# Optimization experiments

Hardware: AMD Instinct MI355X
Metric: run time of the kernel (lower is better)

## Reference

```python
import jax, jax.numpy as jnp
import numpy as np

B, L, H, HEADS = 2, 2048, 1024, 16
D = H // HEADS  # head_dim = 64


def _rel_pos_bias(q, pos_emb):
    """Skewing trick: q is (b,h,L,d) (already scaled), pos_emb is (2L-1,d).
    Returns relative positional bias of shape (b,h,L,L)."""
    b, h, l, _ = q.shape
    p = jnp.einsum('bhid,jd->bhij', q, pos_emb)          # (b,h,L,2L-1)
    p = jnp.pad(p, ((0, 0), (0, 0), (0, 0), (0, 1)))     # (b,h,L,2L)
    p = p.reshape(b, h, l * 2 * l)                        # flatten last two dims
    p = jnp.pad(p, ((0, 0), (0, 0), (0, l - 1)))          # append L-1 zeros
    p = p.reshape(b, h, l + 1, 2 * l - 1)
    return p[:, :, :-1, -l:]                              # (b,h,L,L)


def setup_inputs() -> dict:
    key = jax.random.key(0)
    ks = jax.random.split(key, 12)
    s = 1.0 / np.sqrt(H)
    inp = {
        'query': jax.random.normal(ks[0], (B, L, H), jnp.float32),
        'key':   jax.random.normal(ks[1], (B, L, H), jnp.float32),
        'value': jax.random.normal(ks[2], (B, L, H), jnp.float32),
        'Wq_w': jax.random.normal(ks[3], (H, H), jnp.float32) * s,
        'Wq_b': jnp.zeros((H,), jnp.float32),
        'Wk_w': jax.random.normal(ks[4], (H, H), jnp.float32) * s,
        'Wk_b': jnp.zeros((H,), jnp.float32),
        'Wv_w': jax.random.normal(ks[5], (H, H), jnp.float32) * s,
        'Wv_b': jnp.zeros((H,), jnp.float32),
        'Wo_w': jax.random.normal(ks[6], (H, H), jnp.float32) * s,
        'Wo_b': jnp.zeros((H,), jnp.float32),
        'pos_emb': jax.random.normal(ks[7], (2 * L - 1, D), jnp.float32),
    }
    return inp


def reference(query, key, value, Wq_w, Wq_b, Wk_w, Wk_b, Wv_w, Wv_b, Wo_w, Wo_b, pos_emb):
    b = query.shape[0]
    q = query @ Wq_w.T + Wq_b
    k = key @ Wk_w.T + Wk_b
    v = value @ Wv_w.T + Wv_b
    # (b,L,h*d) -> (b,h,L,d)
    split = lambda x: x.reshape(b, L, HEADS, D).transpose(0, 2, 1, 3)
    q, k, v = split(q), split(k), split(v)
    q = q / np.sqrt(D)  # note: scaled q is also used for positional bias (faithful)
    attn = jnp.einsum('bhid,bhjd->bhij', q, k)
    attn = attn + _rel_pos_bias(q, pos_emb)
    causal = jnp.triu(jnp.full((L, L), -jnp.inf, jnp.float32), k=1)
    attn = attn + causal  # broadcasts over (b,h)
    score = jax.nn.softmax(attn, axis=-1)
    out = jnp.einsum('bhqk,bhkd->bhqd', score, v)
    out = out.transpose(0, 2, 1, 3).reshape(b, L, H)
    return out @ Wo_w.T + Wo_b
```

## Files before the change

### kernel.cpp

```cpp
#include <hip/hip_runtime.h>

#define L_SEQ 2048
#define NH    16
#define HD    64
#define HDIM  1024

typedef __attribute__((ext_vector_type(8))) short  short8;
typedef __attribute__((ext_vector_type(4))) float  f32x4;

__device__ __forceinline__ unsigned short f2bf(float f) {
    unsigned int u = __float_as_uint(f);
    u += 0x7fffu + ((u >> 16) & 1u);
    return (unsigned short)(u >> 16);
}

__device__ __forceinline__ short8 ld8(const unsigned short* p) {
    return *(const short8*)p;
}

__device__ __forceinline__ unsigned int cvtpk(float a, float b) {
    unsigned int r;
    asm("v_cvt_pk_bf16_f32 %0, %1, %2" : "=v"(r) : "v"(a), "v"(b));
    return r;
}

__device__ __forceinline__ void gl16(const unsigned short* g, unsigned short* l) {
    __builtin_amdgcn_global_load_lds(
        (const __attribute__((address_space(1))) void*)g,
        (__attribute__((address_space(3))) void*)l, 16, 0, 0);
}

__global__ __launch_bounds__(256) void cvt_a_kernel(
    const float* __restrict__ q, const float* __restrict__ k,
    const float* __restrict__ Wq, const float* __restrict__ Wk,
    const float* __restrict__ Wv, const float* __restrict__ Wo,
    const float* __restrict__ pe,
    unsigned short* __restrict__ S1, unsigned short* __restrict__ Vb,
    unsigned short* __restrict__ D, unsigned short* __restrict__ E)
{
    const int y = blockIdx.y;
    const float* src; unsigned short* dst; int n8;
    switch (y) {
        case 0:  src = q;  dst = S1;            n8 = 524288; break;
        case 1:  src = k;  dst = Vb;            n8 = 524288; break;
        case 2:  src = Wq; dst = D;             n8 = 131072; break;
        case 3:  src = Wk; dst = D + 1048576;   n8 = 131072; break;
        case 4:  src = Wv; dst = D + 2097152;   n8 = 131072; break;
        case 5:  src = Wo; dst = D + 3145728;   n8 = 131072; break;
        default: src = pe; dst = E;             n8 = 32760;  break;
    }
    const int i = blockIdx.x * 256 + threadIdx.x;
    if (i >= n8) return;
    const float4 a = ((const float4*)src)[2 * i];
    const float4 b = ((const float4*)src)[2 * i + 1];
    union { short8 v; unsigned int u[4]; } o;
    o.u[0] = cvtpk(a.x, a.y); o.u[1] = cvtpk(a.z, a.w);
    o.u[2] = cvtpk(b.x, b.y); o.u[3] = cvtpk(b.z, b.w);
    ((short8*)dst)[i] = o.v;
}

__global__ __launch_bounds__(256) void cvt_x_kernel(const float* __restrict__ src,
                                                    unsigned short* __restrict__ dst) {
    const int i = blockIdx.x * 256 + threadIdx.x;
    const float4 a = ((const float4*)src)[2 * i];
    const float4 b = ((const float4*)src)[2 * i + 1];
    union { short8 v; unsigned int u[4]; } o;
    o.u[0] = cvtpk(a.x, a.y); o.u[1] = cvtpk(a.z, a.w);
    o.u[2] = cvtpk(b.x, b.y); o.u[3] = cvtpk(b.z, b.w);
    ((short8*)dst)[i] = o.v;
}

__device__ __forceinline__ void gemm_bf16_core(
    const unsigned short* __restrict__ Xb,
    const unsigned short* __restrict__ Wb,
    int row0, int col0,
    unsigned short* As, unsigned short* Bs,
    f32x4 (&acc)[4][4])
{
    const int t    = threadIdx.x;
    const int lane = t & 63;
    const int wid  = t >> 6;
    const int lr   = lane & 15;
    const int lg   = lane >> 4;
    const int wr   = (wid >> 1) << 6;
    const int wc   = (wid & 1) << 6;

    const int grow = lane >> 3;
    const int gcol = ((lane & 7) ^ grow) << 3;

#pragma unroll
    for (int m = 0; m < 4; ++m)
#pragma unroll
        for (int n = 0; n < 4; ++n)
            acc[m][n] = (f32x4)0.0f;

    const unsigned short* xs = Xb + (size_t)(row0 + grow) * 1024 + gcol;
    const unsigned short* ws = Wb + (size_t)(col0 + grow) * 1024 + gcol;

    for (int k0 = 0; k0 < 1024; k0 += 64) {
        __syncthreads();
#pragma unroll
        for (int i = 0; i < 4; ++i) {
            const int seg = (i << 2) + wid;
            gl16(xs + (size_t)(seg << 3) * 1024 + k0, As + seg * 512);
            gl16(ws + (size_t)(seg << 3) * 1024 + k0, Bs + seg * 512);
        }
        __syncthreads();

        short8 af[4][2], bf[4][2];
#pragma unroll
        for (int m = 0; m < 4; ++m) {
            const int row = wr + (m << 4) + lr;
#pragma unroll
            for (int h = 0; h < 2; ++h)
                af[m][h] = ld8(&As[row * 64 + ((((h << 2) + lg) ^ (lr & 7)) << 3)]);
        }
#pragma unroll
        for (int n = 0; n < 4; ++n) {
            const int row = wc + (n << 4) + lr;
#pragma unroll
            for (int h = 0; h < 2; ++h)
                bf[n][h] = ld8(&Bs[row * 64 + ((((h << 2) + lg) ^ (lr & 7)) << 3)]);
        }
#pragma unroll
        for (int m = 0; m < 4; ++m)
#pragma unroll
            for (int n = 0; n < 4; ++n) {
                acc[m][n] = __builtin_amdgcn_mfma_f32_16x16x32_bf16(af[m][0], bf[n][0], acc[m][n], 0, 0, 0);
                acc[m][n] = __builtin_amdgcn_mfma_f32_16x16x32_bf16(af[m][1], bf[n][1], acc[m][n], 0, 0, 0);
            }
    }
}

__global__ __launch_bounds__(256) void proj_qk_kernel(
    const unsigned short* __restrict__ Xq, const unsigned short* __restrict__ Xk,
    const unsigned short* __restrict__ D,
    const float* __restrict__ bq, const float* __restrict__ bk,
    unsigned short* __restrict__ Qb, unsigned short* __restrict__ Kb)
{
    __shared__ __align__(16) unsigned short As[128 * 64];
    __shared__ __align__(16) unsigned short Bs[128 * 64];

    const int z = blockIdx.x >> 8;
    const int d = blockIdx.x & 255;
    const int y = ((d >> 6) << 3) | (d & 7);
    const int x = (d >> 3) & 7;
    const int row0 = y << 7, col0 = x << 7;

    const unsigned short* Xb = z ? Xk : Xq;
    const unsigned short* Wb = D + (z ? 1048576 : 0);
    const float* bias = z ? bk : bq;
    unsigned short* out = z ? Kb : Qb;
    const float scale = z ? 1.0f : 0.125f;

    f32x4 acc[4][4];
    gemm_bf16_core(Xb, Wb, row0, col0, As, Bs, acc);

    const int t = threadIdx.x;
    const int lane = t & 63;
    const int wid  = t >> 6;
    const int lr = lane & 15, lg = lane >> 4;
    const int wr = (wid >> 1) << 6, wc = (wid & 1) << 6;

#pragma unroll
    for (int n = 0; n < 4; ++n) {
        const int o = col0 + wc + (n << 4) + lr;
        const float bo = bias[o];
        const int h = o >> 6, dd = o & 63;
#pragma unroll
        for (int m = 0; m < 4; ++m) {
            const int ib = row0 + wr + (m << 4) + (lg << 2);
#pragma unroll
            for (int r = 0; r < 4; ++r) {
                const int i = ib + r;
                out[(((size_t)((i >> 11) * NH + h)) * L_SEQ + (i & (L_SEQ - 1))) * HD + dd] =
                    f2bf((acc[m][n][r] + bo) * scale);
            }
        }
    }
}

__global__ __launch_bounds__(256) void proj_v_kernel(
    const unsigned short* __restrict__ Xb, const unsigned short* __restrict__ Wb,
    const float* __restrict__ bias, unsigned short* __restrict__ out)
{
    __shared__ __align__(16) unsigned short As[128 * 64];
    __shared__ __align__(16) unsigned short Bs[128 * 64];

    const int d = blockIdx.x;
    const int y = ((d >> 6) << 3) | (d & 7);
    const int x = (d >> 3) & 7;
    const int row0 = y << 7, col0 = x << 7;

    f32x4 acc[4][4];
    gemm_bf16_core(Xb, Wb, row0, col0, As, Bs, acc);

    const int t = threadIdx.x;
    const int lane = t & 63;
    const int wid  = t >> 6;
    const int lr = lane & 15, lg = lane >> 4;
    const int wr = (wid >> 1) << 6, wc = (wid & 1) << 6;

#pragma unroll
    for (int n = 0; n < 4; ++n) {
        const int o = col0 + wc + (n << 4) + lr;
        const float bo = bias[o];
        const int h = o >> 6, dd = o & 63;
#pragma unroll
        for (int m = 0; m < 4; ++m) {
            const int ib = row0 + wr + (m << 4) + (lg << 2);
            const int b = ib >> 11, il = ib & (L_SEQ - 1);
            ushort4 pk;
            pk.x = f2bf(acc[m][n][0] + bo);
            pk.y = f2bf(acc[m][n][1] + bo);
            pk.z = f2bf(acc[m][n][2] + bo);
            pk.w = f2bf(acc[m][n][3] + bo);
            *(ushort4*)&out[(((size_t)(b * NH + h)) * HD + dd) * L_SEQ + il] = pk;
        }
    }
}

__global__ __launch_bounds__(256) void outproj_kernel(
    const unsigned short* __restrict__ Ob, const unsigned short* __restrict__ Wb,
    const float* __restrict__ bias, float* __restrict__ Yout)
{
    __shared__ __align__(16) unsigned short As[128 * 64];
    __shared__ __align__(16) unsigned short Bs[128 * 64];

    const int d = blockIdx.x;
    const int y = ((d >> 6) << 3) | (d & 7);
    const int x = (d >> 3) & 7;
    const int row0 = y << 7, col0 = x << 7;

    f32x4 acc[4][4];
    gemm_bf16_core(Ob, Wb, row0, col0, As, Bs, acc);

    const int t = threadIdx.x;
    const int lane = t & 63;
    const int wid  = t >> 6;
    const int lr = lane & 15, lg = lane >> 4;
    const int wr = (wid >> 1) << 6, wc = (wid & 1) << 6;

#pragma unroll
    for (int n = 0; n < 4; ++n) {
        const int o = col0 + wc + (n << 4) + lr;
        const float bo = bias[o];
#pragma unroll
        for (int m = 0; m < 4; ++m) {
            const int ib = row0 + wr + (m << 4) + (lg << 2);
#pragma unroll
            for (int r = 0; r < 4; ++r)
                Yout[(size_t)(ib + r) * HDIM + o] = acc[m][n][r] + bo;
        }
    }
}

__device__ __forceinline__ void stage_kv(
    const unsigned short* __restrict__ kbase, const unsigned short* __restrict__ vbase,
    int j0, unsigned short (*Ksb)[64], unsigned short (*Vsb)[64], int wid, int lane)
{
    const int r8 = lane >> 3;
    const int gc = ((lane & 7) ^ r8) << 3;
#pragma unroll
    for (int s = 0; s < 2; ++s) {
        const int rw = (wid << 4) + (s << 3);
        gl16(kbase + (size_t)(j0 + rw + r8) * HD + gc, &Ksb[rw][0]);
        gl16(vbase + (size_t)(rw + r8) * L_SEQ + j0 + gc, &Vsb[rw][0]);
    }
}

__global__ __launch_bounds__(256, 3) void attn_kernel(
    const unsigned short* __restrict__ Q,
    const unsigned short* __restrict__ Kt,
    const unsigned short* __restrict__ VT,
    const unsigned short* __restrict__ PE,
    unsigned short* __restrict__ O)
{
    __shared__ __align__(16) unsigned short Ks[2][64][64];
    __shared__ __align__(16) unsigned short Vs[2][64][64];
    __shared__ __align__(16) float blds_all[4][64][20];

    const int t    = threadIdx.x;
    const int wid  = t >> 6;
    const int lane = t & 63;
    const int lr   = lane & 15;
    const int lg   = lane >> 4;
    const int lk   = lg << 3;

    const int p   = blockIdx.x;
    const int bh  = p & 31;
    const int rb  = 31 - (p >> 5);
    const int i0  = rb << 6;
    const int i0w = i0 + (wid << 4);
    const int nt  = rb + 1;

    const unsigned short* kbase = Kt + (size_t)bh * L_SEQ * HD;
    const unsigned short* vbase = VT + (size_t)bh * HD * L_SEQ;

    float (*blds)[20] = blds_all[wid];

    const unsigned short* qb = Q + ((size_t)bh * L_SEQ + i0w + lr) * HD + lk;
    const short8 aq0 = ld8(qb);
    const short8 aq1 = ld8(qb + 32);

    const int gi    = i0w + lr;
    const int idx0  = ((lg & 1) << 7) + (lr << 2);
    const int idx1  = idx0 + 64;
    const int selhi = lg >> 1;

    f32x4 oacc[4];
#pragma unroll
    for (int dt = 0; dt < 4; ++dt) oacc[dt] = (f32x4)0.0f;
    float mrun = -__builtin_inff();
    float lrun = 0.0f;

    const int jend = i0w + 15;

    f32x4 pqc = (f32x4)0.0f;
    {
        const unsigned short* pp = PE + (size_t)(2032 - i0w + lr) * HD + lk;
        pqc = __builtin_amdgcn_mfma_f32_16x16x32_bf16(aq0, ld8(pp), pqc, 0, 0, 0);
        pqc = __builtin_amdgcn_mfma_f32_16x16x32_bf16(aq1, ld8(pp + 32), pqc, 0, 0, 0);
    }

    stage_kv(kbase, vbase, 0, Ks[0], Vs[0], wid, lane);
    __syncthreads();

    int cur = 0;
    for (int tt = 0; tt < nt; ++tt) {
        const int j0   = tt << 6;
        const bool more = (tt + 1 < nt);

        if (more)
            stage_kv(kbase, vbase, j0 + 64, Ks[cur ^ 1], Vs[cur ^ 1], wid, lane);

        if (j0 <= jend) {
            f32x4 s2[4];
#pragma unroll
            for (int ct = 0; ct < 4; ++ct) {
                const int row = (ct << 4) + lr;
                const short8 k0 = *(const short8*)&Ks[cur][row][(lg ^ (lr & 7)) << 3];
                const short8 k1 = *(const short8*)&Ks[cur][row][((4 + lg) ^ (lr & 7)) << 3];
                f32x4 a = (f32x4)0.0f;
                a = __builtin_amdgcn_mfma_f32_16x16x32_bf16(k0, aq0, a, 0, 0, 0);
                a = __builtin_amdgcn_mfma_f32_16x16x32_bf16(k1, aq1, a, 0, 0, 0);
                s2[ct] = a;
            }

            const int mlo = 2032 + j0 - i0w;
            f32x4 pq[5];
            pq[0] = pqc;
#pragma unroll
            for (int pt = 1; pt < 5; ++pt) {
                f32x4 a = (f32x4)0.0f;
                const unsigned short* pp = PE + (size_t)(mlo + (pt << 4) + lr) * HD + lk;
                a = __builtin_amdgcn_mfma_f32_16x16x32_bf16(aq0, ld8(pp), a, 0, 0, 0);
                a = __builtin_amdgcn_mfma_f32_16x16x32_bf16(aq1, ld8(pp + 32), a, 0, 0, 0);
                pq[pt] = a;
            }
            pqc = pq[4];

#pragma unroll
            for (int r = 0; r < 4; ++r) {
                const int qw = (lg << 2) + r;
                {
                    const int kr = lr + qw - 15;
                    if (kr >= 0) blds[kr][qw] = pq[0][r];
                }
#pragma unroll
                for (int pt = 1; pt < 4; ++pt)
                    blds[(pt << 4) + lr + qw - 15][qw] = pq[pt][r];
                {
                    const int kr = 49 + lr + qw;
                    if (kr < 64) blds[kr][qw] = pq[4][r];
                }
            }

#pragma unroll
            for (int ct = 0; ct < 4; ++ct)
#pragma unroll
                for (int r = 0; r < 4; ++r) {
                    const int krl = (ct << 4) + (lg << 2) + r;
                    const float v = s2[ct][r] + blds[krl][lr];
                    s2[ct][r] = (j0 + krl > gi) ? -__builtin_inff() : v;
                }

            float c0 = fmaxf(fmaxf(s2[0][0], s2[0][1]), fmaxf(s2[0][2], s2[0][3]));
            float c1 = fmaxf(fmaxf(s2[1][0], s2[1][1]), fmaxf(s2[1][2], s2[1][3]));
            float c2 = fmaxf(fmaxf(s2[2][0], s2[2][1]), fmaxf(s2[2][2], s2[2][3]));
            float c3 = fmaxf(fmaxf(s2[3][0], s2[3][1]), fmaxf(s2[3][2], s2[3][3]));
            float vmax = fmaxf(fmaxf(c0, c1), fmaxf(c2, c3));
            vmax = fmaxf(vmax, __shfl_xor(vmax, 16));
            vmax = fmaxf(vmax, __shfl_xor(vmax, 32));
            const float mnew = fmaxf(mrun, vmax);
            const float sc = __expf(mrun - mnew);
            mrun = mnew;
#pragma unroll
            for (int ct = 0; ct < 4; ++ct)
#pragma unroll
                for (int r = 0; r < 4; ++r)
                    s2[ct][r] = __expf(s2[ct][r] - mnew);
            float t0 = (s2[0][0] + s2[0][1]) + (s2[0][2] + s2[0][3]);
            float t1 = (s2[1][0] + s2[1][1]) + (s2[1][2] + s2[1][3]);
            float t2 = (s2[2][0] + s2[2][1]) + (s2[2][2] + s2[2][3]);
            float t3 = (s2[3][0] + s2[3][1]) + (s2[3][2] + s2[3][3]);
            float sum = (t0 + t1) + (t2 + t3);
            sum += __shfl_xor(sum, 16);
            sum += __shfl_xor(sum, 32);
            lrun = lrun * sc + sum;
#pragma unroll
            for (int dt = 0; dt < 4; ++dt)
#pragma unroll
                for (int r = 0; r < 4; ++r)
                    oacc[dt][r] *= sc;

            unsigned int pkl[4], pkh[4];
#pragma unroll
            for (int ct = 0; ct < 4; ++ct) {
                pkl[ct] = cvtpk(s2[ct][0], s2[ct][1]);
                pkh[ct] = cvtpk(s2[ct][2], s2[ct][3]);
            }
            union { short8 v; int u[4]; } pf0, pf1;
#pragma unroll
            for (int m = 0; m < 4; ++m) {
                const int bidx = (m & 2) ? idx1 : idx0;
                const int a0 = __builtin_amdgcn_ds_bpermute(bidx, (int)((m & 1) ? pkh[0] : pkl[0]));
                const int a1 = __builtin_amdgcn_ds_bpermute(bidx, (int)((m & 1) ? pkh[1] : pkl[1]));
                pf0.u[m] = selhi ? a1 : a0;
                const int b0 = __builtin_amdgcn_ds_bpermute(bidx, (int)((m & 1) ? pkh[2] : pkl[2]));
                const int b1 = __builtin_amdgcn_ds_bpermute(bidx, (int)((m & 1) ? pkh[3] : pkl[3]));
                pf1.u[m] = selhi ? b1 : b0;
            }

#pragma unroll
            for (int dt = 0; dt < 4; ++dt) {
                const int row = (dt << 4) + lr;
                const short8 v0 = *(const short8*)&Vs[cur][row][(lg ^ (lr & 7)) << 3];
                const short8 v1 = *(const short8*)&Vs[cur][row][((4 + lg) ^ (lr & 7)) << 3];
                oacc[dt] = __builtin_amdgcn_mfma_f32_16x16x32_bf16(v0, pf0.v, oacc[dt], 0, 0, 0);
                oacc[dt] = __builtin_amdgcn_mfma_f32_16x16x32_bf16(v1, pf1.v, oacc[dt], 0, 0, 0);
            }
        }

        __syncthreads();
        cur ^= 1;
    }

    const float inv = 1.0f / lrun;
    const int b = bh >> 4, h = bh & 15;
#pragma unroll
    for (int dt = 0; dt < 4; ++dt) {
        uint2 u;
        u.x = cvtpk(oacc[dt][0] * inv, oacc[dt][1] * inv);
        u.y = cvtpk(oacc[dt][2] * inv, oacc[dt][3] * inv);
        *(uint2*)&O[((size_t)b * L_SEQ + i0w + lr) * HDIM + (h << 6) + (dt << 4) + (lg << 2)] = u;
    }
}

extern "C" void kernel_launch(void* const* d_in, const int* in_sizes, int n_in,
                              void* d_out, int out_size, void* d_ws, size_t ws_size,
                              hipStream_t stream) {
    (void)in_sizes; (void)n_in; (void)out_size;

    const float* query   = (const float*)d_in[0];
    const float* key_    = (const float*)d_in[1];
    const float* value   = (const float*)d_in[2];
    const float* Wq_w    = (const float*)d_in[3];
    const float* Wq_b    = (const float*)d_in[4];
    const float* Wk_w    = (const float*)d_in[5];
    const float* Wk_b    = (const float*)d_in[6];
    const float* Wv_w    = (const float*)d_in[7];
    const float* Wv_b    = (const float*)d_in[8];
    const float* Wo_w    = (const float*)d_in[9];
    const float* Wo_b    = (const float*)d_in[10];
    const float* pos_emb = (const float*)d_in[11];

    char* ws = (char*)d_ws;
    const size_t MB = 1024 * 1024;
    unsigned short* S1 = (unsigned short*)(ws);
    unsigned short* Qb = (unsigned short*)(ws + 8  * MB);
    unsigned short* Kb = (unsigned short*)(ws + 16 * MB);
    unsigned short* Vb = (unsigned short*)(ws + 24 * MB);
    unsigned short* D  = (unsigned short*)(ws + 32 * MB);
    unsigned short* E  = (unsigned short*)(ws + 40 * MB);

    const int npe = (2 * L_SEQ - 1) * HD;
    if (ws_size < (size_t)40 * MB + (size_t)npe * 2) return;

    cvt_a_kernel<<<dim3(2048, 7), 256, 0, stream>>>(query, key_, Wq_w, Wk_w, Wv_w, Wo_w,
                                                    pos_emb, S1, Vb, D, E);
    proj_qk_kernel<<<512, 256, 0, stream>>>(S1, Vb, D, Wq_b, Wk_b, Qb, Kb);
    cvt_x_kernel<<<2048, 256, 0, stream>>>(value, S1);
    proj_v_kernel<<<256, 256, 0, stream>>>(S1, D + 2097152, Wv_b, Vb);
    attn_kernel<<<1024, 256, 0, stream>>>(Qb, Kb, Vb, E, S1);
    outproj_kernel<<<256, 256, 0, stream>>>(S1, D + 3145728, Wo_b, (float*)d_out);
}
```

Measured before the change: 179.5 us.

## Fuse V projection into QK launch, add lazy softmax rescale and exp2

The value-input conversion is folded into the main conversion launch and the V projection into the Q/K projection launch. This removes two kernel launches and lets the three GEMMs fill the device together, using the output buffer as scratch for bf16 V and transposed V. In attention, Q is prescaled by log2(e) so the softmax uses exp2. The running-max rescale is skipped unless the max grows by more than a threshold, and the causal mask is applied only on diagonal tiles. The lazy rescale relies on fp32 headroom and adds a wave-wide vote.

```diff
diff --git a/kernel.cpp b/kernel.cpp
--- a/kernel.cpp
+++ b/kernel.cpp
@@ -31,11 +31,12 @@
 }
 
 __global__ __launch_bounds__(256) void cvt_a_kernel(
-    const float* __restrict__ q, const float* __restrict__ k,
+    const float* __restrict__ q, const float* __restrict__ k, const float* __restrict__ v,
     const float* __restrict__ Wq, const float* __restrict__ Wk,
     const float* __restrict__ Wv, const float* __restrict__ Wo,
     const float* __restrict__ pe,
     unsigned short* __restrict__ S1, unsigned short* __restrict__ Vb,
+    unsigned short* __restrict__ VSCR,
     unsigned short* __restrict__ D, unsigned short* __restrict__ E)
 {
     const int y = blockIdx.y;
@@ -47,7 +48,8 @@
         case 3:  src = Wk; dst = D + 1048576;   n8 = 131072; break;
         case 4:  src = Wv; dst = D + 2097152;   n8 = 131072; break;
         case 5:  src = Wo; dst = D + 3145728;   n8 = 131072; break;
-        default: src = pe; dst = E;             n8 = 32760;  break;
+        case 6:  src = pe; dst = E;             n8 = 32760;  break;
+        default: src = v;  dst = VSCR;          n8 = 524288; break;
     }
     const int i = blockIdx.x * 256 + threadIdx.x;
     if (i >= n8) return;
@@ -59,17 +61,6 @@
     ((short8*)dst)[i] = o.v;
 }
 
-__global__ __launch_bounds__(256) void cvt_x_kernel(const float* __restrict__ src,
-                                                    unsigned short* __restrict__ dst) {
-    const int i = blockIdx.x * 256 + threadIdx.x;
-    const float4 a = ((const float4*)src)[2 * i];
-    const float4 b = ((const float4*)src)[2 * i + 1];
-    union { short8 v; unsigned int u[4]; } o;
-    o.u[0] = cvtpk(a.x, a.y); o.u[1] = cvtpk(a.z, a.w);
-    o.u[2] = cvtpk(b.x, b.y); o.u[3] = cvtpk(b.z, b.w);
-    ((short8*)dst)[i] = o.v;
-}
-
 __device__ __forceinline__ void gemm_bf16_core(
     const unsigned short* __restrict__ Xb,
     const unsigned short* __restrict__ Wb,
@@ -132,11 +123,12 @@
     }
 }
 
-__global__ __launch_bounds__(256) void proj_qk_kernel(
+__global__ __launch_bounds__(256) void proj_qkv_kernel(
     const unsigned short* __restrict__ Xq, const unsigned short* __restrict__ Xk,
-    const unsigned short* __restrict__ D,
-    const float* __restrict__ bq, const float* __restrict__ bk,
-    unsigned short* __restrict__ Qb, unsigned short* __restrict__ Kb)
+    const unsigned short* __restrict__ Xv, const unsigned short* __restrict__ D,
+    const float* __restrict__ bq, const float* __restrict__ bk, const float* __restrict__ bv,
+    unsigned short* __restrict__ Qb, unsigned short* __restrict__ Kb,
+    unsigned short* __restrict__ VT)
 {
     __shared__ __align__(16) unsigned short As[128 * 64];
     __shared__ __align__(16) unsigned short Bs[128 * 64];
@@ -147,11 +139,9 @@
     const int x = (d >> 3) & 7;
     const int row0 = y << 7, col0 = x << 7;
 
-    const unsigned short* Xb = z ? Xk : Xq;
-    const unsigned short* Wb = D + (z ? 1048576 : 0);
-    const float* bias = z ? bk : bq;
-    unsigned short* out = z ? Kb : Qb;
-    const float scale = z ? 1.0f : 0.125f;
+    const unsigned short* Xb = (z == 0) ? Xq : (z == 1) ? Xk : Xv;
+    const unsigned short* Wb = D + (size_t)z * 1048576;
+    const float* bias = (z == 0) ? bq : (z == 1) ? bk : bv;
 
     f32x4 acc[4][4];
     gemm_bf16_core(Xb, Wb, row0, col0, As, Bs, acc);
@@ -162,60 +152,42 @@
     const int lr = lane & 15, lg = lane >> 4;
     const int wr = (wid >> 1) << 6, wc = (wid & 1) << 6;
 
-#pragma unroll
-    for (int n = 0; n < 4; ++n) {
-        const int o = col0 + wc + (n << 4) + lr;
-        const float bo = bias[o];
-        const int h = o >> 6, dd = o & 63;
-#pragma unroll
-        for (int m = 0; m < 4; ++m) {
-            const int ib = row0 + wr + (m << 4) + (lg << 2);
-#pragma unroll
-            for (int r = 0; r < 4; ++r) {
-                const int i = ib + r;
-                out[(((size_t)((i >> 11) * NH + h)) * L_SEQ + (i & (L_SEQ - 1))) * HD + dd] =
-                    f2bf((acc[m][n][r] + bo) * scale);
-            }
-        }
-    }
-}
-
-__global__ __launch_bounds__(256) void proj_v_kernel(
-    const unsigned short* __restrict__ Xb, const unsigned short* __restrict__ Wb,
-    const float* __restrict__ bias, unsigned short* __restrict__ out)
-{
-    __shared__ __align__(16) unsigned short As[128 * 64];
-    __shared__ __align__(16) unsigned short Bs[128 * 64];
-
-    const int d = blockIdx.x;
-    const int y = ((d >> 6) << 3) | (d & 7);
-    const int x = (d >> 3) & 7;
-    const int row0 = y << 7, col0 = x << 7;
-
-    f32x4 acc[4][4];
-    gemm_bf16_core(Xb, Wb, row0, col0, As, Bs, acc);
-
-    const int t = threadIdx.x;
-    const int lane = t & 63;
-    const int wid  = t >> 6;
-    const int lr = lane & 15, lg = lane >> 4;
-    const int wr = (wid >> 1) << 6, wc = (wid & 1) << 6;
-
-#pragma unroll
-    for (int n = 0; n < 4; ++n) {
-        const int o = col0 + wc + (n << 4) + lr;
-        const float bo = bias[o];
-        const int h = o >> 6, dd = o & 63;
-#pragma unroll
-        for (int m = 0; m < 4; ++m) {
-            const int ib = row0 + wr + (m << 4) + (lg << 2);
-            const int b = ib >> 11, il = ib & (L_SEQ - 1);
-            ushort4 pk;
-            pk.x = f2bf(acc[m][n][0] + bo);
-            pk.y = f2bf(acc[m][n][1] + bo);
-            pk.z = f2bf(acc[m][n][2] + bo);
-            pk.w = f2bf(acc[m][n][3] + bo);
-            *(ushort4*)&out[(((size_t)(b * NH + h)) * HD + dd) * L_SEQ + il] = pk;
+    if (z <= 1) {
+        const float scale = (z == 0) ? 0.125f * 1.44269504088896340736f : 1.0f;
+        unsigned short* out = (z == 0) ? Qb : Kb;
+#pragma unroll
+        for (int n = 0; n < 4; ++n) {
+            const int o = col0 + wc + (n << 4) + lr;
+            const float bo = bias[o];
+            const int h = o >> 6, dd = o & 63;
+#pragma unroll
+            for (int m = 0; m < 4; ++m) {
+                const int ib = row0 + wr + (m << 4) + (lg << 2);
+#pragma unroll
+                for (int r = 0; r < 4; ++r) {
+                    const int i = ib + r;
+                    out[(((size_t)((i >> 11) * NH + h)) * L_SEQ + (i & (L_SEQ - 1))) * HD + dd] =
+                        f2bf((acc[m][n][r] + bo) * scale);
+                }
+            }
+        }
+    } else {
+#pragma unroll
+        for (int n = 0; n < 4; ++n) {
+            const int o = col0 + wc + (n << 4) + lr;
+            const float bo = bias[o];
+            const int h = o >> 6, dd = o & 63;
+#pragma unroll
+            for (int m = 0; m < 4; ++m) {
+                const int ib = row0 + wr + (m << 4) + (lg << 2);
+                const int b = ib >> 11, il = ib & (L_SEQ - 1);
+                ushort4 pk;
+                pk.x = f2bf(acc[m][n][0] + bo);
+                pk.y = f2bf(acc[m][n][1] + bo);
+                pk.z = f2bf(acc[m][n][2] + bo);
+                pk.w = f2bf(acc[m][n][3] + bo);
+                *(ushort4*)&VT[(((size_t)(b * NH + h)) * HD + dd) * L_SEQ + il] = pk;
+            }
         }
     }
 }
@@ -376,14 +348,24 @@
                 }
             }
 
-#pragma unroll
-            for (int ct = 0; ct < 4; ++ct)
-#pragma unroll
-                for (int r = 0; r < 4; ++r) {
-                    const int krl = (ct << 4) + (lg << 2) + r;
-                    const float v = s2[ct][r] + blds[krl][lr];
-                    s2[ct][r] = (j0 + krl > gi) ? -__builtin_inff() : v;
-                }
+            if (j0 + 63 > i0w) {
+#pragma unroll
+                for (int ct = 0; ct < 4; ++ct)
+#pragma unroll
+                    for (int r = 0; r < 4; ++r) {
+                        const int krl = (ct << 4) + (lg << 2) + r;
+                        const float v = s2[ct][r] + blds[krl][lr];
+                        s2[ct][r] = (j0 + krl > gi) ? -__builtin_inff() : v;
+                    }
+            } else {
+#pragma unroll
+                for (int ct = 0; ct < 4; ++ct)
+#pragma unroll
+                    for (int r = 0; r < 4; ++r) {
+                        const int krl = (ct << 4) + (lg << 2) + r;
+                        s2[ct][r] += blds[krl][lr];
+                    }
+            }
 
             float c0 = fmaxf(fmaxf(s2[0][0], s2[0][1]), fmaxf(s2[0][2], s2[0][3]));
             float c1 = fmaxf(fmaxf(s2[1][0], s2[1][1]), fmaxf(s2[1][2], s2[1][3]));
@@ -392,14 +374,22 @@
             float vmax = fmaxf(fmaxf(c0, c1), fmaxf(c2, c3));
             vmax = fmaxf(vmax, __shfl_xor(vmax, 16));
             vmax = fmaxf(vmax, __shfl_xor(vmax, 32));
-            const float mnew = fmaxf(mrun, vmax);
-            const float sc = __expf(mrun - mnew);
-            mrun = mnew;
+            if (!__all(vmax <= mrun + 8.0f)) {
+                const float mnew = fmaxf(mrun, vmax);
+                const float sc = __builtin_amdgcn_exp2f(mrun - mnew);
+                mrun = mnew;
+                lrun *= sc;
+#pragma unroll
+                for (int dt = 0; dt < 4; ++dt)
+#pragma unroll
+                    for (int r = 0; r < 4; ++r)
+                        oacc[dt][r] *= sc;
+            }
 #pragma unroll
             for (int ct = 0; ct < 4; ++ct)
 #pragma unroll
                 for (int r = 0; r < 4; ++r)
-                    s2[ct][r] = __expf(s2[ct][r] - mnew);
+                    s2[ct][r] = __builtin_amdgcn_exp2f(s2[ct][r] - mrun);
             float t0 = (s2[0][0] + s2[0][1]) + (s2[0][2] + s2[0][3]);
             float t1 = (s2[1][0] + s2[1][1]) + (s2[1][2] + s2[1][3]);
             float t2 = (s2[2][0] + s2[2][1]) + (s2[2][2] + s2[2][3]);
@@ -407,12 +397,7 @@
             float sum = (t0 + t1) + (t2 + t3);
             sum += __shfl_xor(sum, 16);
             sum += __shfl_xor(sum, 32);
-            lrun = lrun * sc + sum;
-#pragma unroll
-            for (int dt = 0; dt < 4; ++dt)
-#pragma unroll
-                for (int r = 0; r < 4; ++r)
-                    oacc[dt][r] *= sc;
+            lrun += sum;
 
             unsigned int pkl[4], pkh[4];
 #pragma unroll
@@ -484,14 +469,17 @@
     unsigned short* D  = (unsigned short*)(ws + 32 * MB);
     unsigned short* E  = (unsigned short*)(ws + 40 * MB);
 
+    unsigned short* VSCR = (unsigned short*)d_out;
+    unsigned short* VT   = VSCR + 4194304;
+
     const int npe = (2 * L_SEQ - 1) * HD;
     if (ws_size < (size_t)40 * MB + (size_t)npe * 2) return;
 
-    cvt_a_kernel<<<dim3(2048, 7), 256, 0, stream>>>(query, key_, Wq_w, Wk_w, Wv_w, Wo_w,
-                                                    pos_emb, S1, Vb, D, E);
-    proj_qk_kernel<<<512, 256, 0, stream>>>(S1, Vb, D, Wq_b, Wk_b, Qb, Kb);
-    cvt_x_kernel<<<2048, 256, 0, stream>>>(value, S1);
-    proj_v_kernel<<<256, 256, 0, stream>>>(S1, D + 2097152, Wv_b, Vb);
-    attn_kernel<<<1024, 256, 0, stream>>>(Qb, Kb, Vb, E, S1);
+    cvt_a_kernel<<<dim3(2048, 8), 256, 0, stream>>>(query, key_, value,
+                                                    Wq_w, Wk_w, Wv_w, Wo_w, pos_emb,
+                                                    S1, Vb, VSCR, D, E);
+    proj_qkv_kernel<<<768, 256, 0, stream>>>(S1, Vb, VSCR, D, Wq_b, Wk_b, Wv_b,
+                                             Qb, Kb, VT);
+    attn_kernel<<<1024, 256, 0, stream>>>(Qb, Kb, VT, E, S1);
     outproj_kernel<<<256, 256, 0, stream>>>(S1, D + 3145728, Wo_b, (float*)d_out);
 }
```

After: 172.1 us, median of 4. 4.1% less time.
